# Kernel tuning notes

Measured on AMD Instinct MI355X. Metric: run time of the kernel, lower is better.

Reference implementation:

```python
import jax, jax.numpy as jnp
import numpy as np

B, V, D = 256, 4096, 64

def setup_inputs() -> dict:
    key = jax.random.key(0)
    k1, k2 = jax.random.split(key)
    fusion_fs = jax.random.normal(k1, (B, V, D), dtype=jnp.float32)
    lan_fs = jax.random.normal(k2, (B, 1, D), dtype=jnp.float32)
    return {"fusion_fs": fusion_fs, "lan_fs": lan_fs}

def reference(fusion_fs, lan_fs):
    # sim_map: [b, a, q=1, v]
    sim = jnp.einsum('avd,bqd->baqv', fusion_fs, lan_fs)
    top2, _ = jax.lax.top_k(sim, 2)          # [B, B, 1, 2], sorted descending
    top2 = jnp.squeeze(top2, axis=2)          # [B, B, 2]  (q == 1)
    max_sim_0 = top2[..., 0]                  # [B, B]
    max_sim_1 = top2[..., 1]                  # [B, B]
    b = max_sim_0.shape[0]
    # off-diagonal selection of max_sim_1 -> [B, B-1], row-major order
    i = jnp.arange(b)[:, None]
    j = jnp.arange(b - 1)[None, :]
    max_sim_1_off = max_sim_1[i, j + (j >= i)]
    logits = jnp.concatenate([max_sim_0, max_sim_1_off], axis=1)  # [B, 2B-1]
    # target_pred = argmax(eye) = arange(B); CE with mean reduction
    logp = jax.nn.log_softmax(logits, axis=1)
    labels = jnp.arange(b)
    loss = -jnp.mean(logp[labels, labels])
    return loss
```

## Files before the change

### kernel.cpp

```cpp
#include <hip/hip_runtime.h>
#include <math.h>

#define BB 256
#define VV 4096
#define DD 64
#define NCHUNK 32
#define CHB 32768

typedef __attribute__((ext_vector_type(8))) _Float16 f16x8;
typedef __attribute__((ext_vector_type(2))) __fp16 fp16x2;
typedef __attribute__((ext_vector_type(4))) float f32x4;
typedef __attribute__((address_space(3))) void lds_void_t;
typedef const __attribute__((address_space(1))) void gvoid_t;

__global__ __launch_bounds__(512) void topk_sim_kernel(
    const float* __restrict__ F, const float* __restrict__ lan,
    float* __restrict__ max0T, float* __restrict__ max1T)
{
  extern __shared__ __align__(16) char smem[];
  __shared__ float mrg[8][64][2];

  const int t = threadIdx.x;
  const int a = blockIdx.x;
  const int wave = t >> 6;
  const int lane = t & 63;
  const int cl = lane & 15;
  const int o  = lane >> 4;
  const int rg = wave >> 2;
  const int cg = wave & 3;

  const char* gFa = (const char*)(F + (size_t)a * VV * DD);

  int soff[4];
#pragma unroll
  for (int i = 0; i < 4; ++i) {
    int row = wave * 16 + i * 4 + o;
    soff[i] = row * 256 + (cl ^ (row & 7)) * 16;
  }

  auto stage = [&](int ch, char* buf) {
    const char* g = gFa + (size_t)ch * CHB;
    char* dst = buf + wave * 4096;
#pragma unroll
    for (int i = 0; i < 4; ++i) {
      __builtin_amdgcn_global_load_lds(
          (gvoid_t*)(g + soff[i]),
          (lds_void_t*)(dst + i * 1024), 16, 0, 0);
    }
  };

  stage(0, smem);
  stage(1, smem + CHB);

  f16x8 bf[4][2];
#pragma unroll
  for (int ct = 0; ct < 4; ++ct)
#pragma unroll
    for (int s = 0; s < 2; ++s) {
      const float* p = lan + (cg * 64 + ct * 16 + cl) * DD + s * 32 + o * 8;
      float4 u0 = *(const float4*)p, u1 = *(const float4*)(p + 4);
      union { f16x8 v; fp16x2 h[4]; } U;
      U.h[0] = __builtin_amdgcn_cvt_pkrtz(u0.x, u0.y);
      U.h[1] = __builtin_amdgcn_cvt_pkrtz(u0.z, u0.w);
      U.h[2] = __builtin_amdgcn_cvt_pkrtz(u1.x, u1.y);
      U.h[3] = __builtin_amdgcn_cvt_pkrtz(u1.z, u1.w);
      bf[ct][s] = U.v;
    }

  float m0[4], m1[4];
#pragma unroll
  for (int ct = 0; ct < 4; ++ct) { m0[ct] = -INFINITY; m1[ct] = -INFINITY; }

  auto compute = [&](const char* buf) {
#pragma unroll
    for (int rt = 0; rt < 4; ++rt) {
      const int row = rg * 64 + rt * 16 + cl;
      const int rx = row & 7;
      const char* rp = buf + row * 256;
      float4 u00 = *(const float4*)(rp + ((((o * 2 + 0) ^ rx)) << 4));
      float4 u01 = *(const float4*)(rp + ((((o * 2 + 1) ^ rx)) << 4));
      float4 u10 = *(const float4*)(rp + ((8 + ((o * 2 + 0) ^ rx)) << 4));
      float4 u11 = *(const float4*)(rp + ((8 + ((o * 2 + 1) ^ rx)) << 4));
      union { f16x8 v; fp16x2 h[4]; } A0, A1;
      A0.h[0] = __builtin_amdgcn_cvt_pkrtz(u00.x, u00.y);
      A0.h[1] = __builtin_amdgcn_cvt_pkrtz(u00.z, u00.w);
      A0.h[2] = __builtin_amdgcn_cvt_pkrtz(u01.x, u01.y);
      A0.h[3] = __builtin_amdgcn_cvt_pkrtz(u01.z, u01.w);
      A1.h[0] = __builtin_amdgcn_cvt_pkrtz(u10.x, u10.y);
      A1.h[1] = __builtin_amdgcn_cvt_pkrtz(u10.z, u10.w);
      A1.h[2] = __builtin_amdgcn_cvt_pkrtz(u11.x, u11.y);
      A1.h[3] = __builtin_amdgcn_cvt_pkrtz(u11.z, u11.w);
#pragma unroll
      for (int ct = 0; ct < 4; ++ct) {
        f32x4 acc = {0.f, 0.f, 0.f, 0.f};
        acc = __builtin_amdgcn_mfma_f32_16x16x32_f16(A0.v, bf[ct][0], acc, 0, 0, 0);
        acc = __builtin_amdgcn_mfma_f32_16x16x32_f16(A1.v, bf[ct][1], acc, 0, 0, 0);
        float h1 = fmaxf(acc[0], acc[1]), q1 = fminf(acc[0], acc[1]);
        float h2 = fmaxf(acc[2], acc[3]), q2 = fminf(acc[2], acc[3]);
        float M0 = fmaxf(h1, h2);
        float M1 = fmaxf(fminf(h1, h2), fmaxf(q1, q2));
        float old0 = m0[ct];
        m0[ct] = fmaxf(old0, M0);
        m1[ct] = fmaxf(m1[ct], fmaxf(fminf(old0, M0), M1));
      }
    }
  };

#pragma unroll 1
  for (int ch = 0; ch < NCHUNK; ++ch) {
    if (ch + 2 < NCHUNK) {
      stage(ch + 2, smem + (size_t)((ch + 2) & 3) * CHB);
      asm volatile("s_waitcnt vmcnt(8)" ::: "memory");
    } else if (ch + 1 < NCHUNK) {
      asm volatile("s_waitcnt vmcnt(4)" ::: "memory");
    } else {
      asm volatile("s_waitcnt vmcnt(0)" ::: "memory");
    }
    __builtin_amdgcn_s_barrier();
    __builtin_amdgcn_sched_barrier(0);
    compute(smem + (size_t)(ch & 3) * CHB);
  }

#pragma unroll
  for (int ct = 0; ct < 4; ++ct) {
#pragma unroll
    for (int off = 16; off <= 32; off <<= 1) {
      float p0 = __shfl_xor(m0[ct], off);
      float p1 = __shfl_xor(m1[ct], off);
      float n1 = fmaxf(fminf(m0[ct], p0), fmaxf(m1[ct], p1));
      m0[ct] = fmaxf(m0[ct], p0);
      m1[ct] = n1;
    }
    if (lane < 16) {
      mrg[wave][ct * 16 + lane][0] = m0[ct];
      mrg[wave][ct * 16 + lane][1] = m1[ct];
    }
  }
  __syncthreads();

  if (t < BB) {
    const int cg2 = t >> 6, lc = t & 63;
    float a0 = mrg[cg2][lc][0],     a1 = mrg[cg2][lc][1];
    float b0 = mrg[4 + cg2][lc][0], b1 = mrg[4 + cg2][lc][1];
    float M0 = fmaxf(a0, b0);
    float M1 = fmaxf(fminf(a0, b0), fmaxf(a1, b1));
    max0T[a * BB + t] = M0;
    max1T[a * BB + t] = M1;
  }
}

__global__ __launch_bounds__(256) void lse_kernel(
    const float* __restrict__ max0T, const float* __restrict__ max1T,
    float* __restrict__ lossb)
{
  __shared__ float red[256];
  __shared__ float diag;
  const int b = blockIdx.x;
  const int t = threadIdx.x;
  float x0 = max0T[t * BB + b];
  float x1 = (t == b) ? -INFINITY : max1T[t * BB + b];
  if (t == b) diag = x0;
  red[t] = fmaxf(x0, x1);
  __syncthreads();
  for (int s = 128; s > 0; s >>= 1) {
    if (t < s) red[t] = fmaxf(red[t], red[t + s]);
    __syncthreads();
  }
  float M = red[0];
  __syncthreads();
  float e = expf(x0 - M) + ((t == b) ? 0.0f : expf(x1 - M));
  red[t] = e;
  __syncthreads();
  for (int s = 128; s > 0; s >>= 1) {
    if (t < s) red[t] = red[t] + red[t + s];
    __syncthreads();
  }
  if (t == 0) lossb[b] = logf(red[0]) + M - diag;
}

__global__ __launch_bounds__(256) void mean_kernel(
    const float* __restrict__ lossb, float* __restrict__ out)
{
  __shared__ float red[256];
  const int t = threadIdx.x;
  red[t] = lossb[t];
  __syncthreads();
  for (int s = 128; s > 0; s >>= 1) {
    if (t < s) red[t] += red[t + s];
    __syncthreads();
  }
  if (t == 0) out[0] = red[0] * (1.0f / 256.0f);
}

extern "C" void kernel_launch(void* const* d_in, const int* in_sizes, int n_in,
                              void* d_out, int out_size, void* d_ws, size_t ws_size,
                              hipStream_t stream) {
  const float* F   = (const float*)d_in[0];
  const float* lan = (const float*)d_in[1];
  float* ws = (float*)d_ws;
  float* max0T = ws;
  float* max1T = ws + 65536;
  float* lossb = ws + 131072;

  const int shmem = 4 * CHB;
  hipFuncSetAttribute((const void*)topk_sim_kernel,
                      hipFuncAttributeMaxDynamicSharedMemorySize, shmem);
  topk_sim_kernel<<<256, 512, shmem, stream>>>(F, lan, max0T, max1T);
  lse_kernel<<<256, 256, 0, stream>>>(max0T, max1T, lossb);
  mean_kernel<<<1, 256, 0, stream>>>(lossb, (float*)d_out);
}
```

Baseline: 72.01 us.

## Deepen global-to-LDS prefetch pipeline with smaller chunks and eight-slot ring

```diff
diff --git a/kernel.cpp b/kernel.cpp
--- a/kernel.cpp
+++ b/kernel.cpp
@@ -4,8 +4,9 @@
 #define BB 256
 #define VV 4096
 #define DD 64
-#define NCHUNK 32
-#define CHB 32768
+#define NCHUNK 64
+#define CHB 16384
+#define DEPTH 6
 
 typedef __attribute__((ext_vector_type(8))) _Float16 f16x8;
 typedef __attribute__((ext_vector_type(2))) __fp16 fp16x2;
@@ -31,39 +32,47 @@
 
   const char* gFa = (const char*)(F + (size_t)a * VV * DD);
 
-  int soff[4];
-#pragma unroll
-  for (int i = 0; i < 4; ++i) {
-    int row = wave * 16 + i * 4 + o;
+  int soff[2];
+#pragma unroll
+  for (int i = 0; i < 2; ++i) {
+    int row = wave * 8 + i * 4 + o;
     soff[i] = row * 256 + (cl ^ (row & 7)) * 16;
   }
 
   auto stage = [&](int ch, char* buf) {
     const char* g = gFa + (size_t)ch * CHB;
-    char* dst = buf + wave * 4096;
-#pragma unroll
-    for (int i = 0; i < 4; ++i) {
+    char* dst = buf + wave * 2048;
+#pragma unroll
+    for (int i = 0; i < 2; ++i) {
       __builtin_amdgcn_global_load_lds(
           (gvoid_t*)(g + soff[i]),
           (lds_void_t*)(dst + i * 1024), 16, 0, 0);
     }
   };
 
-  stage(0, smem);
-  stage(1, smem + CHB);
-
-  f16x8 bf[4][2];
+  float4 bu[4][2][2];
 #pragma unroll
   for (int ct = 0; ct < 4; ++ct)
 #pragma unroll
     for (int s = 0; s < 2; ++s) {
       const float* p = lan + (cg * 64 + ct * 16 + cl) * DD + s * 32 + o * 8;
-      float4 u0 = *(const float4*)p, u1 = *(const float4*)(p + 4);
+      bu[ct][s][0] = *(const float4*)p;
+      bu[ct][s][1] = *(const float4*)(p + 4);
+    }
+
+#pragma unroll
+  for (int i = 0; i < DEPTH; ++i) stage(i, smem + (size_t)i * CHB);
+
+  f16x8 bf[4][2];
+#pragma unroll
+  for (int ct = 0; ct < 4; ++ct)
+#pragma unroll
+    for (int s = 0; s < 2; ++s) {
       union { f16x8 v; fp16x2 h[4]; } U;
-      U.h[0] = __builtin_amdgcn_cvt_pkrtz(u0.x, u0.y);
-      U.h[1] = __builtin_amdgcn_cvt_pkrtz(u0.z, u0.w);
-      U.h[2] = __builtin_amdgcn_cvt_pkrtz(u1.x, u1.y);
-      U.h[3] = __builtin_amdgcn_cvt_pkrtz(u1.z, u1.w);
+      U.h[0] = __builtin_amdgcn_cvt_pkrtz(bu[ct][s][0].x, bu[ct][s][0].y);
+      U.h[1] = __builtin_amdgcn_cvt_pkrtz(bu[ct][s][0].z, bu[ct][s][0].w);
+      U.h[2] = __builtin_amdgcn_cvt_pkrtz(bu[ct][s][1].x, bu[ct][s][1].y);
+      U.h[3] = __builtin_amdgcn_cvt_pkrtz(bu[ct][s][1].z, bu[ct][s][1].w);
       bf[ct][s] = U.v;
     }
 
@@ -73,8 +82,8 @@
 
   auto compute = [&](const char* buf) {
 #pragma unroll
-    for (int rt = 0; rt < 4; ++rt) {
-      const int row = rg * 64 + rt * 16 + cl;
+    for (int rt = 0; rt < 2; ++rt) {
+      const int row = rg * 32 + rt * 16 + cl;
       const int rx = row & 7;
       const char* rp = buf + row * 256;
       float4 u00 = *(const float4*)(rp + ((((o * 2 + 0) ^ rx)) << 4));
@@ -108,17 +117,21 @@
 
 #pragma unroll 1
   for (int ch = 0; ch < NCHUNK; ++ch) {
-    if (ch + 2 < NCHUNK) {
-      stage(ch + 2, smem + (size_t)((ch + 2) & 3) * CHB);
-      asm volatile("s_waitcnt vmcnt(8)" ::: "memory");
-    } else if (ch + 1 < NCHUNK) {
-      asm volatile("s_waitcnt vmcnt(4)" ::: "memory");
+    if (ch + DEPTH < NCHUNK) {
+      stage(ch + DEPTH, smem + (size_t)((ch + DEPTH) & 7) * CHB);
+      asm volatile("s_waitcnt vmcnt(12)" ::: "memory");
     } else {
-      asm volatile("s_waitcnt vmcnt(0)" ::: "memory");
+      const int rem = NCHUNK - 1 - ch;
+      if (rem >= 5)      asm volatile("s_waitcnt vmcnt(10)" ::: "memory");
+      else if (rem == 4) asm volatile("s_waitcnt vmcnt(8)"  ::: "memory");
+      else if (rem == 3) asm volatile("s_waitcnt vmcnt(6)"  ::: "memory");
+      else if (rem == 2) asm volatile("s_waitcnt vmcnt(4)"  ::: "memory");
+      else if (rem == 1) asm volatile("s_waitcnt vmcnt(2)"  ::: "memory");
+      else               asm volatile("s_waitcnt vmcnt(0)"  ::: "memory");
     }
     __builtin_amdgcn_s_barrier();
     __builtin_amdgcn_sched_barrier(0);
-    compute(smem + (size_t)(ch & 3) * CHB);
+    compute(smem + (size_t)(ch & 7) * CHB);
   }
 
 #pragma unroll
@@ -202,7 +215,7 @@
   float* max1T = ws + 65536;
   float* lossb = ws + 131072;
 
-  const int shmem = 4 * CHB;
+  const int shmem = 8 * CHB;
   hipFuncSetAttribute((const void*)topk_sim_kernel,
                       hipFuncAttributeMaxDynamicSharedMemorySize, shmem);
   topk_sim_kernel<<<256, 512, shmem, stream>>>(F, lan, max0T, max1T);
```

Measured after the change: 77.77 us. 8.0% more time.

## Split each sample's V range across two 256-thread blocks with partial top-2 merge

Applied to the files above, without the earlier changes.

```diff
diff --git a/kernel.cpp b/kernel.cpp
--- a/kernel.cpp
+++ b/kernel.cpp
@@ -5,7 +5,7 @@
 #define VV 4096
 #define DD 64
 #define NCHUNK 32
-#define CHB 32768
+#define CHB 16384
 
 typedef __attribute__((ext_vector_type(8))) _Float16 f16x8;
 typedef __attribute__((ext_vector_type(2))) __fp16 fp16x2;
@@ -13,23 +13,23 @@
 typedef __attribute__((address_space(3))) void lds_void_t;
 typedef const __attribute__((address_space(1))) void gvoid_t;
 
-__global__ __launch_bounds__(512) void topk_sim_kernel(
+__global__ __launch_bounds__(256) void topk_sim_kernel(
     const float* __restrict__ F, const float* __restrict__ lan,
-    float* __restrict__ max0T, float* __restrict__ max1T)
+    float* __restrict__ max0P, float* __restrict__ max1P)
 {
   extern __shared__ __align__(16) char smem[];
-  __shared__ float mrg[8][64][2];
 
   const int t = threadIdx.x;
-  const int a = blockIdx.x;
+  const int a    = blockIdx.x >> 1;
+  const int half = blockIdx.x & 1;
   const int wave = t >> 6;
   const int lane = t & 63;
   const int cl = lane & 15;
   const int o  = lane >> 4;
-  const int rg = wave >> 2;
-  const int cg = wave & 3;
-
-  const char* gFa = (const char*)(F + (size_t)a * VV * DD);
+  const int cg = wave;
+
+  const char* gFa = (const char*)(F + (size_t)a * VV * DD
+                                  + (size_t)half * 2048 * DD);
 
   int soff[4];
 #pragma unroll
@@ -49,6 +49,16 @@
     }
   };
 
+  float4 bu[4][2][2];
+#pragma unroll
+  for (int ct = 0; ct < 4; ++ct)
+#pragma unroll
+    for (int s = 0; s < 2; ++s) {
+      const float* p = lan + (cg * 64 + ct * 16 + cl) * DD + s * 32 + o * 8;
+      bu[ct][s][0] = *(const float4*)p;
+      bu[ct][s][1] = *(const float4*)(p + 4);
+    }
+
   stage(0, smem);
   stage(1, smem + CHB);
 
@@ -57,13 +67,11 @@
   for (int ct = 0; ct < 4; ++ct)
 #pragma unroll
     for (int s = 0; s < 2; ++s) {
-      const float* p = lan + (cg * 64 + ct * 16 + cl) * DD + s * 32 + o * 8;
-      float4 u0 = *(const float4*)p, u1 = *(const float4*)(p + 4);
       union { f16x8 v; fp16x2 h[4]; } U;
-      U.h[0] = __builtin_amdgcn_cvt_pkrtz(u0.x, u0.y);
-      U.h[1] = __builtin_amdgcn_cvt_pkrtz(u0.z, u0.w);
-      U.h[2] = __builtin_amdgcn_cvt_pkrtz(u1.x, u1.y);
-      U.h[3] = __builtin_amdgcn_cvt_pkrtz(u1.z, u1.w);
+      U.h[0] = __builtin_amdgcn_cvt_pkrtz(bu[ct][s][0].x, bu[ct][s][0].y);
+      U.h[1] = __builtin_amdgcn_cvt_pkrtz(bu[ct][s][0].z, bu[ct][s][0].w);
+      U.h[2] = __builtin_amdgcn_cvt_pkrtz(bu[ct][s][1].x, bu[ct][s][1].y);
+      U.h[3] = __builtin_amdgcn_cvt_pkrtz(bu[ct][s][1].z, bu[ct][s][1].w);
       bf[ct][s] = U.v;
     }
 
@@ -74,7 +82,7 @@
   auto compute = [&](const char* buf) {
 #pragma unroll
     for (int rt = 0; rt < 4; ++rt) {
-      const int row = rg * 64 + rt * 16 + cl;
+      const int row = rt * 16 + cl;
       const int rx = row & 7;
       const char* rp = buf + row * 256;
       float4 u00 = *(const float4*)(rp + ((((o * 2 + 0) ^ rx)) << 4));
@@ -132,33 +140,28 @@
       m1[ct] = n1;
     }
     if (lane < 16) {
-      mrg[wave][ct * 16 + lane][0] = m0[ct];
-      mrg[wave][ct * 16 + lane][1] = m1[ct];
-    }
-  }
-  __syncthreads();
-
-  if (t < BB) {
-    const int cg2 = t >> 6, lc = t & 63;
-    float a0 = mrg[cg2][lc][0],     a1 = mrg[cg2][lc][1];
-    float b0 = mrg[4 + cg2][lc][0], b1 = mrg[4 + cg2][lc][1];
-    float M0 = fmaxf(a0, b0);
-    float M1 = fmaxf(fminf(a0, b0), fmaxf(a1, b1));
-    max0T[a * BB + t] = M0;
-    max1T[a * BB + t] = M1;
+      const int col = cg * 64 + ct * 16 + lane;
+      max0P[((size_t)a * 2 + half) * BB + col] = m0[ct];
+      max1P[((size_t)a * 2 + half) * BB + col] = m1[ct];
+    }
   }
 }
 
 __global__ __launch_bounds__(256) void lse_kernel(
-    const float* __restrict__ max0T, const float* __restrict__ max1T,
+    const float* __restrict__ max0P, const float* __restrict__ max1P,
     float* __restrict__ lossb)
 {
   __shared__ float red[256];
   __shared__ float diag;
   const int b = blockIdx.x;
   const int t = threadIdx.x;
-  float x0 = max0T[t * BB + b];
-  float x1 = (t == b) ? -INFINITY : max1T[t * BB + b];
+  float p00 = max0P[((size_t)t * 2 + 0) * BB + b];
+  float p01 = max0P[((size_t)t * 2 + 1) * BB + b];
+  float p10 = max1P[((size_t)t * 2 + 0) * BB + b];
+  float p11 = max1P[((size_t)t * 2 + 1) * BB + b];
+  float x0 = fmaxf(p00, p01);
+  float x1m = fmaxf(fminf(p00, p01), fmaxf(p10, p11));
+  float x1 = (t == b) ? -INFINITY : x1m;
   if (t == b) diag = x0;
   red[t] = fmaxf(x0, x1);
   __syncthreads();
@@ -198,14 +201,14 @@
   const float* F   = (const float*)d_in[0];
   const float* lan = (const float*)d_in[1];
   float* ws = (float*)d_ws;
-  float* max0T = ws;
-  float* max1T = ws + 65536;
-  float* lossb = ws + 131072;
+  float* max0P = ws;
+  float* max1P = ws + 131072;
+  float* lossb = ws + 262144;
 
   const int shmem = 4 * CHB;
   hipFuncSetAttribute((const void*)topk_sim_kernel,
                       hipFuncAttributeMaxDynamicSharedMemorySize, shmem);
-  topk_sim_kernel<<<256, 512, shmem, stream>>>(F, lan, max0T, max1T);
-  lse_kernel<<<256, 256, 0, stream>>>(max0T, max1T, lossb);
+  topk_sim_kernel<<<512, 256, shmem, stream>>>(F, lan, max0P, max1P);
+  lse_kernel<<<256, 256, 0, stream>>>(max0P, max1P, lossb);
   mean_kernel<<<1, 256, 0, stream>>>(lossb, (float*)d_out);
 }
```

After: 78.05 us. 1.08x slower.

## Convert chunks to fp16 once in registers and double-buffer LDS

Applied to the files above, without the earlier changes.

```diff
diff --git a/kernel.cpp b/kernel.cpp
--- a/kernel.cpp
+++ b/kernel.cpp
@@ -5,13 +5,12 @@
 #define VV 4096
 #define DD 64
 #define NCHUNK 32
-#define CHB 32768
+#define CHBG 32768
+#define CHBL 16384
 
 typedef __attribute__((ext_vector_type(8))) _Float16 f16x8;
 typedef __attribute__((ext_vector_type(2))) __fp16 fp16x2;
 typedef __attribute__((ext_vector_type(4))) float f32x4;
-typedef __attribute__((address_space(3))) void lds_void_t;
-typedef const __attribute__((address_space(1))) void gvoid_t;
 
 __global__ __launch_bounds__(512) void topk_sim_kernel(
     const float* __restrict__ F, const float* __restrict__ lan,
@@ -31,41 +30,54 @@
 
   const char* gFa = (const char*)(F + (size_t)a * VV * DD);
 
-  int soff[4];
-#pragma unroll
-  for (int i = 0; i < 4; ++i) {
-    int row = wave * 16 + i * 4 + o;
-    soff[i] = row * 256 + (cl ^ (row & 7)) * 16;
-  }
-
-  auto stage = [&](int ch, char* buf) {
-    const char* g = gFa + (size_t)ch * CHB;
-    char* dst = buf + wave * 4096;
-#pragma unroll
-    for (int i = 0; i < 4; ++i) {
-      __builtin_amdgcn_global_load_lds(
-          (gvoid_t*)(g + soff[i]),
-          (lds_void_t*)(dst + i * 1024), 16, 0, 0);
-    }
-  };
-
-  stage(0, smem);
-  stage(1, smem + CHB);
-
-  f16x8 bf[4][2];
+  float4 bu[4][2][2];
 #pragma unroll
   for (int ct = 0; ct < 4; ++ct)
 #pragma unroll
     for (int s = 0; s < 2; ++s) {
       const float* p = lan + (cg * 64 + ct * 16 + cl) * DD + s * 32 + o * 8;
-      float4 u0 = *(const float4*)p, u1 = *(const float4*)(p + 4);
+      bu[ct][s][0] = *(const float4*)p;
+      bu[ct][s][1] = *(const float4*)(p + 4);
+    }
+  f16x8 bf[4][2];
+#pragma unroll
+  for (int ct = 0; ct < 4; ++ct)
+#pragma unroll
+    for (int s = 0; s < 2; ++s) {
       union { f16x8 v; fp16x2 h[4]; } U;
-      U.h[0] = __builtin_amdgcn_cvt_pkrtz(u0.x, u0.y);
-      U.h[1] = __builtin_amdgcn_cvt_pkrtz(u0.z, u0.w);
-      U.h[2] = __builtin_amdgcn_cvt_pkrtz(u1.x, u1.y);
-      U.h[3] = __builtin_amdgcn_cvt_pkrtz(u1.z, u1.w);
+      U.h[0] = __builtin_amdgcn_cvt_pkrtz(bu[ct][s][0].x, bu[ct][s][0].y);
+      U.h[1] = __builtin_amdgcn_cvt_pkrtz(bu[ct][s][0].z, bu[ct][s][0].w);
+      U.h[2] = __builtin_amdgcn_cvt_pkrtz(bu[ct][s][1].x, bu[ct][s][1].y);
+      U.h[3] = __builtin_amdgcn_cvt_pkrtz(bu[ct][s][1].z, bu[ct][s][1].w);
       bf[ct][s] = U.v;
     }
+
+  const int woff = ((((t & 15) >> 1) ^ ((t >> 4) & 7)) << 4) + (t & 1) * 8;
+  const int wrow = (t >> 4) * 128;
+
+#define LOADG(S0, S1, S2, S3, CH) {                                   \
+    const char* _g = gFa + (size_t)(CH) * CHBG + 16 * t;              \
+    S0 = *(const float4*)(_g);                                        \
+    S1 = *(const float4*)(_g + 8192);                                 \
+    S2 = *(const float4*)(_g + 16384);                                \
+    S3 = *(const float4*)(_g + 24576); }
+
+#define CVTW(S0, S1, S2, S3, BUFP) {                                  \
+    char* _b = (BUFP) + wrow + woff;                                  \
+    uint2 _w;                                                         \
+    union { uint2 u; fp16x2 h[2]; } _c;                               \
+    _c.h[0] = __builtin_amdgcn_cvt_pkrtz(S0.x, S0.y);                 \
+    _c.h[1] = __builtin_amdgcn_cvt_pkrtz(S0.z, S0.w); _w = _c.u;      \
+    *(uint2*)(_b) = _w;                                               \
+    _c.h[0] = __builtin_amdgcn_cvt_pkrtz(S1.x, S1.y);                 \
+    _c.h[1] = __builtin_amdgcn_cvt_pkrtz(S1.z, S1.w); _w = _c.u;      \
+    *(uint2*)(_b + 4096) = _w;                                        \
+    _c.h[0] = __builtin_amdgcn_cvt_pkrtz(S2.x, S2.y);                 \
+    _c.h[1] = __builtin_amdgcn_cvt_pkrtz(S2.z, S2.w); _w = _c.u;      \
+    *(uint2*)(_b + 8192) = _w;                                        \
+    _c.h[0] = __builtin_amdgcn_cvt_pkrtz(S3.x, S3.y);                 \
+    _c.h[1] = __builtin_amdgcn_cvt_pkrtz(S3.z, S3.w); _w = _c.u;      \
+    *(uint2*)(_b + 12288) = _w; }
 
   float m0[4], m1[4];
 #pragma unroll
@@ -75,26 +87,15 @@
 #pragma unroll
     for (int rt = 0; rt < 4; ++rt) {
       const int row = rg * 64 + rt * 16 + cl;
-      const int rx = row & 7;
-      const char* rp = buf + row * 256;
-      float4 u00 = *(const float4*)(rp + ((((o * 2 + 0) ^ rx)) << 4));
-      float4 u01 = *(const float4*)(rp + ((((o * 2 + 1) ^ rx)) << 4));
-      float4 u10 = *(const float4*)(rp + ((8 + ((o * 2 + 0) ^ rx)) << 4));
-      float4 u11 = *(const float4*)(rp + ((8 + ((o * 2 + 1) ^ rx)) << 4));
-      union { f16x8 v; fp16x2 h[4]; } A0, A1;
-      A0.h[0] = __builtin_amdgcn_cvt_pkrtz(u00.x, u00.y);
-      A0.h[1] = __builtin_amdgcn_cvt_pkrtz(u00.z, u00.w);
-      A0.h[2] = __builtin_amdgcn_cvt_pkrtz(u01.x, u01.y);
-      A0.h[3] = __builtin_amdgcn_cvt_pkrtz(u01.z, u01.w);
-      A1.h[0] = __builtin_amdgcn_cvt_pkrtz(u10.x, u10.y);
-      A1.h[1] = __builtin_amdgcn_cvt_pkrtz(u10.z, u10.w);
-      A1.h[2] = __builtin_amdgcn_cvt_pkrtz(u11.x, u11.y);
-      A1.h[3] = __builtin_amdgcn_cvt_pkrtz(u11.z, u11.w);
+      const int rx = cl & 7;
+      const char* lp = buf + row * 128;
+      f16x8 a0 = *(const f16x8*)(lp + ((o ^ rx) << 4));
+      f16x8 a1 = *(const f16x8*)(lp + (((4 + o) ^ rx) << 4));
 #pragma unroll
       for (int ct = 0; ct < 4; ++ct) {
         f32x4 acc = {0.f, 0.f, 0.f, 0.f};
-        acc = __builtin_amdgcn_mfma_f32_16x16x32_f16(A0.v, bf[ct][0], acc, 0, 0, 0);
-        acc = __builtin_amdgcn_mfma_f32_16x16x32_f16(A1.v, bf[ct][1], acc, 0, 0, 0);
+        acc = __builtin_amdgcn_mfma_f32_16x16x32_f16(a0, bf[ct][0], acc, 0, 0, 0);
+        acc = __builtin_amdgcn_mfma_f32_16x16x32_f16(a1, bf[ct][1], acc, 0, 0, 0);
         float h1 = fmaxf(acc[0], acc[1]), q1 = fminf(acc[0], acc[1]);
         float h2 = fmaxf(acc[2], acc[3]), q2 = fminf(acc[2], acc[3]);
         float M0 = fmaxf(h1, h2);
@@ -106,20 +107,44 @@
     }
   };
 
+  char* buf0 = smem;
+  char* buf1 = smem + CHBL;
+
+  float4 E0, E1, E2, E3, O0, O1, O2, O3;
+  LOADG(E0, E1, E2, E3, 0)
+  LOADG(O0, O1, O2, O3, 1)
+  asm volatile("s_waitcnt vmcnt(4)" ::: "memory");
+  CVTW(E0, E1, E2, E3, buf0)
+  asm volatile("s_waitcnt lgkmcnt(0)" ::: "memory");
+  __builtin_amdgcn_s_barrier();
+
 #pragma unroll 1
-  for (int ch = 0; ch < NCHUNK; ++ch) {
-    if (ch + 2 < NCHUNK) {
-      stage(ch + 2, smem + (size_t)((ch + 2) & 3) * CHB);
-      asm volatile("s_waitcnt vmcnt(8)" ::: "memory");
-    } else if (ch + 1 < NCHUNK) {
-      asm volatile("s_waitcnt vmcnt(4)" ::: "memory");
-    } else {
-      asm volatile("s_waitcnt vmcnt(0)" ::: "memory");
-    }
+  for (int q = 0; q < 15; ++q) {
+    const int ch = 2 * q;
+    LOADG(E0, E1, E2, E3, ch + 2)
+    asm volatile("s_waitcnt vmcnt(4)" ::: "memory");
+    __builtin_amdgcn_sched_barrier(0);
+    CVTW(O0, O1, O2, O3, buf1)
+    compute(buf0);
+    asm volatile("s_waitcnt lgkmcnt(0)" ::: "memory");
     __builtin_amdgcn_s_barrier();
+    LOADG(O0, O1, O2, O3, ch + 3)
+    asm volatile("s_waitcnt vmcnt(4)" ::: "memory");
     __builtin_amdgcn_sched_barrier(0);
-    compute(smem + (size_t)(ch & 3) * CHB);
-  }
+    CVTW(E0, E1, E2, E3, buf0)
+    compute(buf1);
+    asm volatile("s_waitcnt lgkmcnt(0)" ::: "memory");
+    __builtin_amdgcn_s_barrier();
+  }
+  asm volatile("s_waitcnt vmcnt(0)" ::: "memory");
+  __builtin_amdgcn_sched_barrier(0);
+  CVTW(O0, O1, O2, O3, buf1)
+  compute(buf0);
+  asm volatile("s_waitcnt lgkmcnt(0)" ::: "memory");
+  __builtin_amdgcn_s_barrier();
+  compute(buf1);
+#undef LOADG
+#undef CVTW
 
 #pragma unroll
   for (int ct = 0; ct < 4; ++ct) {
@@ -202,9 +227,7 @@
   float* max1T = ws + 65536;
   float* lossb = ws + 131072;
 
-  const int shmem = 4 * CHB;
-  hipFuncSetAttribute((const void*)topk_sim_kernel,
-                      hipFuncAttributeMaxDynamicSharedMemorySize, shmem);
+  const int shmem = 2 * CHBL;
   topk_sim_kernel<<<256, 512, shmem, stream>>>(F, lan, max0T, max1T);
   lse_kernel<<<256, 256, 0, stream>>>(max0T, max1T, lossb);
   mean_kernel<<<1, 256, 0, stream>>>(lossb, (float*)d_out);
```

Measured after the change: 66.80 us (median of 2 runs). 7.2% less time.
